# Optimization experiments

Measured on AMD Instinct MI355X. Metric: run time of the kernel, lower is better.

The kernel has to match this reference:

```python
import jax, jax.numpy as jnp
import numpy as np

LEVELS = 256          # 8-bit fake quant, quant_levels=256 in forward
SLM_CUTOFF = 0.05     # lower bound of the SLM LUT (file-loaded in original)
EPS = 1e-8


def _stats(t, pct):
    # QuantizeStats first-calibration-step semantics:
    # max = percentile(t, pct); min = t.min() if >= 0 else -max
    mx = jnp.percentile(t, pct)
    mn = jnp.min(t)
    mn = jnp.where(mn >= 0.0, mn, -mx)
    return jax.lax.stop_gradient(mn), jax.lax.stop_gradient(mx)


def _fake_quant_det(x, mn, mx, lut_min=None):
    diff = mx - mn
    q = jnp.clip(x, mn, mx)
    q = (q - mn) / (diff + EPS) * (LEVELS - 1)
    q = jnp.round(q) / (LEVELS - 1) * diff + mn
    if lut_min is not None:
        # clip positive part up to lut_min*max, negative part down to -lut_min*|min|
        pos = jax.nn.relu(q)
        neg = q - pos
        lms_p = lut_min * mx
        pos = jnp.where(pos < lms_p, lms_p, pos)
        lms_n = lut_min * jnp.abs(mn)
        neg = jnp.where(neg > -lms_n, -lms_n, neg)
        q = pos + neg
    # straight-through estimator (QuantizeValue.backward passes grad through)
    return x + jax.lax.stop_gradient(q - x)


def _fake_quant_rand(x, mn, mx, key):
    diff = mx - mn
    q = jnp.clip(x, mn, mx)
    q = (q - mn) / (diff + EPS) * (LEVELS - 1)
    noise = jax.random.uniform(key, q.shape, q.dtype) - 0.5  # stochastic rounding
    q = jnp.round(q + noise) / (LEVELS - 1) * diff + mn
    return x + jax.lax.stop_gradient(q - x)


def setup_inputs() -> dict:
    key = jax.random.key(0)
    kx, ky = jax.random.split(key)
    x = jax.random.normal(kx, (2, 4, 2048, 64), dtype=jnp.float32)
    y = jax.random.normal(ky, (2, 4, 64, 2048), dtype=jnp.float32)
    return {"x": x, "y": y}


def reference(x, y):
    # QuantizedMatmul.forward, quantize=True, training path
    x_min, x_max = _stats(x, 99.99)
    y_min, y_max = _stats(y, 98.0)
    xq = _fake_quant_det(x, x_min, x_max)
    yq = _fake_quant_det(y, y_min, y_max, SLM_CUTOFF)
    out = jnp.matmul(xq, yq)           # [B,H,M,N]
    o_min, o_max = _stats(out, 99.9999)
    return _fake_quant_rand(out, o_min, o_max, jax.random.key(1))
```

## Files before the change

### kernel.cpp

```cpp
#include <hip/hip_runtime.h>
#include <math.h>

#define CAP  (1u<<20)
#define LCAP 12288
#define LBUF 4096

typedef __attribute__((ext_vector_type(4))) float f32x4;
typedef __attribute__((ext_vector_type(8))) __bf16 bf16x8;
typedef __attribute__((ext_vector_type(8))) unsigned short u16x8;
typedef __attribute__((ext_vector_type(4))) unsigned short u16x4;

__device__ __forceinline__ unsigned f2key(float f){
  unsigned u = __float_as_uint(f);
  return (u & 0x80000000u) ? ~u : (u | 0x80000000u);
}
__device__ __forceinline__ float key2f(unsigned k){
  unsigned u = (k & 0x80000000u) ? (k & 0x7fffffffu) : ~k;
  return __uint_as_float(u);
}
__device__ __forceinline__ unsigned short f2bf(float f){
  unsigned u = __float_as_uint(f);
  u += 0x7FFFu + ((u>>16)&1u);
  return (unsigned short)(u>>16);
}

__device__ __forceinline__ void stage_bf16_tiles(
    const unsigned short* __restrict__ xq, const unsigned short* __restrict__ yqT,
    unsigned short* As, unsigned short* Bs, int brow, int bcol, int tid){
  #pragma unroll
  for (int i=0;i<4;i++){
    int u = tid + i*256;
    int row = u >> 3, ko = (u & 7) << 3;
    u16x8 v = *(const u16x8*)&xq[(size_t)(brow+row)*64 + ko];
    unsigned slot = ((unsigned)(ko>>3)) ^ ((unsigned)row & 7u);
    *(u16x8*)&As[(unsigned)row*64u + slot*8u] = v;
  }
  #pragma unroll
  for (int i=0;i<4;i++){
    int u = tid + i*256;
    int col = u >> 3, ko = (u & 7) << 3;
    u16x8 v = *(const u16x8*)&yqT[(size_t)(bcol+col)*64 + ko];
    unsigned slot = ((unsigned)(ko>>3)) ^ ((unsigned)col & 7u);
    *(u16x8*)&Bs[(unsigned)col*64u + slot*8u] = v;
  }
}

__device__ __forceinline__ void mfma_tile(
    const unsigned short* As, const unsigned short* Bs,
    f32x4 acc[2][8], int w, int lr, int lg){
  #pragma unroll
  for (int kk=0; kk<2; ++kk){
    bf16x8 a[2], bb[8];
    #pragma unroll
    for (int rt=0;rt<2;rt++){
      int row = w*32 + rt*16 + lr;
      unsigned slot = (unsigned)(kk*4 + lg) ^ ((unsigned)row & 7u);
      a[rt] = __builtin_bit_cast(bf16x8, *(const u16x8*)&As[(unsigned)row*64u + slot*8u]);
    }
    #pragma unroll
    for (int ct=0;ct<8;ct++){
      int col = ct*16 + lr;
      unsigned slot = (unsigned)(kk*4 + lg) ^ ((unsigned)col & 7u);
      bb[ct] = __builtin_bit_cast(bf16x8, *(const u16x8*)&Bs[(unsigned)col*64u + slot*8u]);
    }
    #pragma unroll
    for (int rt=0;rt<2;rt++)
      #pragma unroll
      for (int ct=0;ct<8;ct++)
        acc[rt][ct] = __builtin_amdgcn_mfma_f32_16x16x32_bf16(a[rt], bb[ct], acc[rt][ct], 0, 0, 0);
  }
}

__global__ void init_kernel(unsigned* ctrl){
  int tid = blockIdx.x*blockDim.x + threadIdx.x;
  int stride = gridDim.x*blockDim.x;
  for (int i=tid;i<8192;i+=stride) ctrl[i]=0u;
  if (tid<16) ctrl[12291+tid]=0u;
  if (tid>=16 && tid<19) ctrl[12288+(tid-16)]=0xFFFFFFFFu;
}

__global__ __launch_bounds__(256) void hist2_kernel(
    const float4* __restrict__ dA, const float4* __restrict__ dB, int n4A, int n4B,
    unsigned* __restrict__ hA, unsigned* __restrict__ hB,
    unsigned* __restrict__ mkA, unsigned* __restrict__ mkB){
  const int z = blockIdx.y;
  const float4* __restrict__ data = z ? dB : dA;
  const int n4 = z ? n4B : n4A;
  unsigned* hist = z ? hB : hA;
  unsigned* minKey = z ? mkB : mkA;
  __shared__ unsigned sh[8*4096];
  int tid = threadIdx.x;
  for (int i=tid;i<8*4096;i+=blockDim.x) sh[i]=0u;
  __syncthreads();
  const unsigned p = (unsigned)(tid & 7);
  const unsigned cp = p << 12;
  const unsigned rot = p << 2;
  unsigned lmin=0xFFFFFFFFu;
  int idx = blockIdx.x*blockDim.x + tid;
  int stride = gridDim.x*blockDim.x;
  for (int i=idx;i<n4;i+=stride){
    float4 v = data[i];
    unsigned k0=f2key(v.x), k1=f2key(v.y), k2=f2key(v.z), k3=f2key(v.w);
    atomicAdd(&sh[cp + (((k0>>20)+rot)&4095u)],1u);
    atomicAdd(&sh[cp + (((k1>>20)+rot)&4095u)],1u);
    atomicAdd(&sh[cp + (((k2>>20)+rot)&4095u)],1u);
    atomicAdd(&sh[cp + (((k3>>20)+rot)&4095u)],1u);
    lmin = min(lmin, min(min(k0,k1),min(k2,k3)));
  }
  #pragma unroll
  for (int off=32; off; off>>=1) lmin = min(lmin, __shfl_xor(lmin, off));
  if ((tid&63)==0) atomicMin(minKey, lmin);
  __syncthreads();
  for (int i=tid;i<4096;i+=blockDim.x){
    unsigned c=0;
    #pragma unroll
    for (int q=0;q<8;q++) c += sh[(q<<12) + (((unsigned)i + (q<<2))&4095u)];
    if(c) atomicAdd(&hist[i],c);
  }
}

__global__ __launch_bounds__(256) void collect2_kernel(
    const float4* __restrict__ dA, const float4* __restrict__ dB, int n4A, int n4B,
    const unsigned* __restrict__ hA, const unsigned* __restrict__ hB,
    unsigned k1A, unsigned k2A, unsigned k1B, unsigned k2B,
    float* __restrict__ candA, float* __restrict__ candB,
    unsigned* __restrict__ cntA, unsigned* __restrict__ cntB){
  const int z = blockIdx.y;
  const float4* __restrict__ data = z ? dB : dA;
  const int n4 = z ? n4B : n4A;
  const unsigned* __restrict__ hist = z ? hB : hA;
  const unsigned k1 = z ? k1B : k1A;
  const unsigned k2 = z ? k2B : k2A;
  float* cand = z ? candB : candA;
  unsigned* cnt = z ? cntB : cntA;
  __shared__ float sc[LBUF];
  __shared__ unsigned part[256];
  __shared__ unsigned sBi[2];
  __shared__ unsigned scnt, sbase;
  const int t = threadIdx.x;
  if (t==0) scnt=0u;
  unsigned h[16]; unsigned s=0;
  #pragma unroll
  for (int i=0;i<16;i++){ h[i] = hist[t*16+i]; s += h[i]; }
  part[t] = s;
  __syncthreads();
  for (int off=1; off<256; off<<=1){
    unsigned add = (t+off<256) ? part[t+off] : 0u;
    __syncthreads();
    part[t] += add;
    __syncthreads();
  }
  unsigned cum = (t<255) ? part[t+1] : 0u;
  for (int i=15;i>=0;--i){
    unsigned hh = h[i];
    unsigned b = (unsigned)(t*16+i);
    if (cum < k1 && cum + hh >= k1){ sBi[1] = b; }
    if (cum < k2 && cum + hh >= k2){ sBi[0] = b; }
    cum += hh;
  }
  __syncthreads();
  const unsigned blo = sBi[0], bhi = sBi[1];
  int idx = blockIdx.x*blockDim.x + t;
  int stride = gridDim.x*blockDim.x;
  for (int i=idx;i<n4;i+=stride){
    float4 v = data[i];
    float r[4] = {v.x,v.y,v.z,v.w};
    #pragma unroll
    for (int j=0;j<4;j++){
      unsigned b = f2key(r[j]) >> 20;
      if (b>=blo && b<=bhi){
        unsigned p = atomicAdd(&scnt,1u);
        if (p < LBUF) sc[p] = r[j];
        else { unsigned g = atomicAdd(cnt,1u); if (g<CAP) cand[g]=r[j]; }
      }
    }
  }
  __syncthreads();
  unsigned c = scnt; if (c > LBUF) c = LBUF;
  if (t==0 && c>0) sbase = atomicAdd(cnt, c);
  __syncthreads();
  for (unsigned i=t; i<c; i+=256){
    unsigned g = sbase + i;
    if (g < CAP) cand[g] = sc[i];
  }
}

__global__ __launch_bounds__(1024) void select2_kernel(
    const float* __restrict__ candA, const float* __restrict__ candB,
    const unsigned* __restrict__ cntA, const unsigned* __restrict__ cntB,
    const unsigned* __restrict__ hA, const unsigned* __restrict__ hB,
    const unsigned* __restrict__ mkA, const unsigned* __restrict__ mkB,
    unsigned k1A, unsigned k2A, unsigned k1B, unsigned k2B,
    double fracA, double fracB,
    float* __restrict__ stA, float* __restrict__ stB){
  const int z = blockIdx.x;
  const float* __restrict__ cand = z ? candB : candA;
  const unsigned* cnt = z ? cntB : cntA;
  const unsigned* __restrict__ hist_g = z ? hB : hA;
  const unsigned* mk  = z ? mkB  : mkA;
  const unsigned k1 = z ? k1B : k1A;
  const unsigned k2 = z ? k2B : k2A;
  const double frac = z ? fracB : fracA;
  float* stats = z ? stB : stA;

  __shared__ unsigned keys[LCAP];
  __shared__ unsigned histP[16*258];
  __shared__ unsigned hist[256];
  __shared__ unsigned part[256];
  __shared__ unsigned sAbove;
  __shared__ unsigned sPrefix, sK;
  __shared__ unsigned sKey[2];
  const int t = threadIdx.x;
  unsigned m = *cnt; if (m > CAP) m = CAP;
  for (unsigned i=t; i<m && i<LCAP; i+=1024) keys[i] = f2key(cand[i]);

  if (t==0) sAbove = 0u;
  if (hist_g){
    unsigned h[16]; unsigned s=0;
    if (t<256){
      #pragma unroll
      for (int i=0;i<16;i++){ h[i] = hist_g[t*16+i]; s += h[i]; }
      part[t] = s;
    }
    __syncthreads();
    for (int off=1; off<256; off<<=1){
      unsigned add = (t<256 && t+off<256) ? part[t+off] : 0u;
      __syncthreads();
      if (t<256) part[t] += add;
      __syncthreads();
    }
    if (t<256){
      unsigned cum = (t<255) ? part[t+1] : 0u;
      for (int i=15;i>=0;--i){
        unsigned hh = h[i];
        if (cum < k1 && cum + hh >= k1){ sAbove = cum; }
        cum += hh;
      }
    }
  }
  __syncthreads();
  const unsigned above = sAbove;

  for (int tg=0; tg<2; ++tg){
    unsigned k = ((tg==0) ? k1 : k2) - above;
    unsigned prefix = 0u, pmask = 0u;
    for (int s=24; s>=0; s-=8){
      for (int i=t;i<16*258;i+=1024) histP[i]=0u;
      __syncthreads();
      const unsigned base = (unsigned)(t & 15) * 258u;
      for (unsigned i=t;i<m;i+=1024){
        unsigned key = (i<LCAP) ? keys[i] : f2key(cand[i]);
        if ((key & pmask) == prefix) atomicAdd(&histP[base + ((key>>s)&255u)],1u);
      }
      __syncthreads();
      if (t<256){
        unsigned c=0;
        #pragma unroll
        for (int q=0;q<16;q++) c += histP[(unsigned)q*258u + (unsigned)t];
        hist[t] = c;
      }
      __syncthreads();
      if (t<64){
        unsigned h0=hist[t*4+0], h1=hist[t*4+1], h2=hist[t*4+2], h3=hist[t*4+3];
        unsigned g = h0+h1+h2+h3;
        unsigned acc = g;
        #pragma unroll
        for (int off=1; off<64; off<<=1){
          unsigned v = __shfl_down(acc, off);
          acc += (t+off<64) ? v : 0u;
        }
        unsigned ca3 = acc - g;
        unsigned ca2 = ca3 + h3;
        unsigned ca1 = ca2 + h2;
        unsigned ca0 = ca1 + h1;
        if (ca3<k && ca3+h3>=k){ sPrefix = prefix | ((unsigned)(4*t+3)<<s); sK = k-ca3; }
        if (ca2<k && ca2+h2>=k){ sPrefix = prefix | ((unsigned)(4*t+2)<<s); sK = k-ca2; }
        if (ca1<k && ca1+h1>=k){ sPrefix = prefix | ((unsigned)(4*t+1)<<s); sK = k-ca1; }
        if (ca0<k && ca0+h0>=k){ sPrefix = prefix | ((unsigned)(4*t+0)<<s); sK = k-ca0; }
      }
      __syncthreads();
      prefix = sPrefix;
      pmask |= (255u << s);
      k = sK;
    }
    if (t==0) sKey[tg] = prefix;
    __syncthreads();
  }
  if (t==0){
    float vhi = key2f(sKey[0]);
    float vlo = key2f(sKey[1]);
    double mx = (double)vlo + frac * ((double)vhi - (double)vlo);
    float mxf = (float)mx;
    float mnraw = key2f(*mk);
    float mnf = (mnraw >= 0.0f) ? mnraw : -mxf;
    stats[0]=mnf; stats[1]=mxf;
  }
}

__global__ __launch_bounds__(256) void prep_quant_kernel(
    const float4* __restrict__ x, const float* __restrict__ y,
    unsigned short* __restrict__ xq, unsigned short* __restrict__ yqT,
    int n4x, const float* __restrict__ stA, const float* __restrict__ stB){
  if (blockIdx.y == 0){
    const float amn=stA[0], amx=stA[1];
    const float adiff=amx-amn, adenom=adiff+1e-8f;
    int idx = blockIdx.x*256 + threadIdx.x;
    int stride = gridDim.x*256;
    for (int i=idx; i<n4x; i+=stride){
      float4 v = x[i];
      float rr[4]={v.x,v.y,v.z,v.w};
      u16x4 qv;
      #pragma unroll
      for (int j=0;j<4;j++){
        float xv = rr[j];
        float q = fminf(fmaxf(xv, amn), amx);
        q = (q - amn) / adenom * 255.0f;
        q = rintf(q);
        q = q / 255.0f * adiff + amn;
        qv[j] = f2bf(xv + (q - xv));
      }
      *(u16x4*)&xq[(size_t)i*4] = qv;
    }
  } else {
    __shared__ unsigned short Ys[64*72];
    const float bmn=stB[0], bmx=stB[1];
    const float bdiff=bmx-bmn, bdenom=bdiff+1e-8f;
    const float blp=0.05f*bmx, bln=0.05f*fabsf(bmn);
    const int blk = blockIdx.x;
    const int b = blk >> 5, ctile = blk & 31;
    const float* Y = y + (size_t)b*64*2048 + ctile*64;
    const int t = threadIdx.x;
    #pragma unroll
    for (int i=0;i<4;i++){
      int u = t + i*256;
      int k = u >> 4;
      int c4 = (u & 15) << 2;
      float4 v = *(const float4*)&Y[(size_t)k*2048 + c4];
      float rr[4]={v.x,v.y,v.z,v.w};
      #pragma unroll
      for (int j=0;j<4;j++){
        float xv = rr[j];
        float q = fminf(fmaxf(xv, bmn), bmx);
        q = (q - bmn) / bdenom * 255.0f;
        q = rintf(q);
        q = q / 255.0f * bdiff + bmn;
        float pos = fmaxf(q, 0.0f);
        float neg = q - pos;
        pos = (pos < blp) ? blp : pos;
        neg = (neg > -bln) ? -bln : neg;
        q = pos + neg;
        Ys[(c4+j)*72 + k] = f2bf(xv + (q - xv));
      }
    }
    __syncthreads();
    #pragma unroll
    for (int i=0;i<2;i++){
      int u = t + i*256;
      int col = u >> 3, ko = (u & 7) << 3;
      u16x8 v = *(const u16x8*)&Ys[col*72 + ko];
      *(u16x8*)&yqT[((size_t)b*2048 + ctile*64 + col)*64 + ko] = v;
    }
  }
}

__global__ __launch_bounds__(256) void matmul_stats_kernel(
    const unsigned short* __restrict__ xq, const unsigned short* __restrict__ yqT,
    unsigned* __restrict__ bMaxKey, unsigned* __restrict__ bMinKey){
  __shared__ unsigned short As[128*64];
  __shared__ unsigned short Bs[128*64];
  __shared__ float wred[8];
  const int b = blockIdx.z;
  xq  += (size_t)b*2048*64;
  yqT += (size_t)b*2048*64;
  const int brow = blockIdx.y*128, bcol = blockIdx.x*128;
  const int tid = threadIdx.x;
  stage_bf16_tiles(xq, yqT, As, Bs, brow, bcol, tid);
  __syncthreads();
  const int w = tid >> 6, l = tid & 63, lr = l & 15, lg = l >> 4;
  f32x4 zero = {0.f,0.f,0.f,0.f};
  f32x4 acc[2][8];
  #pragma unroll
  for (int rt=0;rt<2;rt++)
    #pragma unroll
    for (int ct=0;ct<8;ct++) acc[rt][ct]=zero;
  mfma_tile(As, Bs, acc, w, lr, lg);
  float tmx = -3.4e38f, tmn = 3.4e38f;
  #pragma unroll
  for (int rt=0;rt<2;rt++)
    #pragma unroll
    for (int ct=0;ct<8;ct++)
      #pragma unroll
      for (int g=0; g<4; g++){
        float v = acc[rt][ct][g];
        tmx = fmaxf(tmx, v);
        tmn = fminf(tmn, v);
      }
  #pragma unroll
  for (int off=32; off; off>>=1){
    tmx = fmaxf(tmx, __shfl_xor(tmx, off));
    tmn = fminf(tmn, __shfl_xor(tmn, off));
  }
  if ((tid&63)==0){ wred[tid>>6]=tmx; wred[4+(tid>>6)]=tmn; }
  __syncthreads();
  if (tid==0){
    float m4 = fmaxf(fmaxf(wred[0],wred[1]),fmaxf(wred[2],wred[3]));
    float n4 = fminf(fminf(wred[4],wred[5]),fminf(wred[6],wred[7]));
    int bid = blockIdx.x + (blockIdx.y<<4) + (blockIdx.z<<8);
    bMaxKey[bid] = f2key(m4);
    bMinKey[bid] = f2key(n4);
  }
}

__global__ __launch_bounds__(256) void thresh_kernel(
    const unsigned* __restrict__ bMaxKey, const unsigned* __restrict__ bMinKey,
    unsigned kth, unsigned* __restrict__ tkey, unsigned* __restrict__ minKeyO){
  __shared__ unsigned red[8];
  const int t = threadIdx.x;
  unsigned kz[8];
  unsigned mn = 0xFFFFFFFFu;
  #pragma unroll
  for (int i=0;i<8;i++){ kz[i] = bMaxKey[t*8+i]; mn = min(mn, bMinKey[t*8+i]); }
  #pragma unroll
  for (int off=32; off; off>>=1) mn = min(mn, __shfl_xor(mn, off));
  if ((t&63)==0) red[4+(t>>6)] = mn;
  __syncthreads();
  if (t==0) *minKeyO = min(min(red[4],red[5]),min(red[6],red[7]));
  unsigned lo=0u, hi=0xFFFFFFFFu;
  while (lo < hi){
    unsigned mid = lo + ((hi-lo)>>1) + 1u;
    unsigned c = 0;
    #pragma unroll
    for (int i=0;i<8;i++) c += (kz[i] >= mid) ? 1u : 0u;
    #pragma unroll
    for (int off=32; off; off>>=1) c += __shfl_xor(c, off);
    __syncthreads();
    if ((t&63)==0) red[t>>6] = c;
    __syncthreads();
    unsigned tot = red[0]+red[1]+red[2]+red[3];
    if (tot >= kth) lo = mid; else hi = mid - 1u;
  }
  if (t==0) *tkey = lo;
}

__global__ __launch_bounds__(256) void collect_tile_kernel(
    const unsigned short* __restrict__ xq, const unsigned short* __restrict__ yqT,
    const unsigned* __restrict__ bMaxKey, const unsigned* __restrict__ tkey,
    float* __restrict__ cand, unsigned* __restrict__ cnt){
  const unsigned T = *tkey;
  const int bid = blockIdx.x + (blockIdx.y<<4) + (blockIdx.z<<8);
  if (bMaxKey[bid] < T) return;
  __shared__ unsigned short As[128*64];
  __shared__ unsigned short Bs[128*64];
  __shared__ float sc[LBUF];
  __shared__ unsigned scnt, sbase;
  const int b = blockIdx.z;
  xq  += (size_t)b*2048*64;
  yqT += (size_t)b*2048*64;
  const int brow = blockIdx.y*128, bcol = blockIdx.x*128;
  const int tid = threadIdx.x;
  if (tid==0) scnt=0u;
  stage_bf16_tiles(xq, yqT, As, Bs, brow, bcol, tid);
  __syncthreads();
  const int w = tid >> 6, l = tid & 63, lr = l & 15, lg = l >> 4;
  f32x4 zero = {0.f,0.f,0.f,0.f};
  f32x4 acc[2][8];
  #pragma unroll
  for (int rt=0;rt<2;rt++)
    #pragma unroll
    for (int ct=0;ct<8;ct++) acc[rt][ct]=zero;
  mfma_tile(As, Bs, acc, w, lr, lg);
  #pragma unroll
  for (int rt=0;rt<2;rt++)
    #pragma unroll
    for (int ct=0;ct<8;ct++)
      #pragma unroll
      for (int g=0; g<4; g++){
        float v = acc[rt][ct][g];
        if (f2key(v) >= T){
          unsigned p = atomicAdd(&scnt,1u);
          if (p < LBUF) sc[p] = v;
          else { unsigned gg = atomicAdd(cnt,1u); if (gg<CAP) cand[gg]=v; }
        }
      }
  __syncthreads();
  unsigned c = scnt; if (c > LBUF) c = LBUF;
  if (tid==0 && c>0) sbase = atomicAdd(cnt, c);
  __syncthreads();
  for (unsigned i=tid; i<c; i+=256){
    unsigned g = sbase + i;
    if (g < CAP) cand[g] = sc[i];
  }
}

__global__ __launch_bounds__(256) void matmul_quant_kernel(
    const unsigned short* __restrict__ xq, const unsigned short* __restrict__ yqT,
    float* __restrict__ C, const float* __restrict__ stO){
  __shared__ unsigned short As[128*64];
  __shared__ unsigned short Bs[128*64];
  const float omn=stO[0], omx=stO[1];
  const float odiff=omx-omn, odenom=odiff+1e-8f;
  const int b = blockIdx.z;
  xq  += (size_t)b*2048*64;
  yqT += (size_t)b*2048*64;
  C   += (size_t)b*2048*2048;
  const int brow = blockIdx.y*128, bcol = blockIdx.x*128;
  const int tid = threadIdx.x;
  stage_bf16_tiles(xq, yqT, As, Bs, brow, bcol, tid);
  __syncthreads();
  const int w = tid >> 6, l = tid & 63, lr = l & 15, lg = l >> 4;
  f32x4 zero = {0.f,0.f,0.f,0.f};
  f32x4 acc[2][8];
  #pragma unroll
  for (int rt=0;rt<2;rt++)
    #pragma unroll
    for (int ct=0;ct<8;ct++) acc[rt][ct]=zero;
  mfma_tile(As, Bs, acc, w, lr, lg);
  #pragma unroll
  for (int rt=0;rt<2;rt++)
    #pragma unroll
    for (int ct=0;ct<8;ct++)
      #pragma unroll
      for (int g=0; g<4; g++){
        float x = acc[rt][ct][g];
        float q = fminf(fmaxf(x, omn), omx);
        q = (q - omn) / odenom * 255.0f;
        q = rintf(q);
        q = q / 255.0f * odiff + omn;
        float v = x + (q - x);
        int row = brow + w*32 + rt*16 + lg*4 + g;
        int col = bcol + ct*16 + lr;
        C[(size_t)row*2048 + col] = v;
      }
}

static void percentile_ranks(long long n, double pct, unsigned& k1, unsigned& k2, double& frac){
  double p = (double)(n - 1) * (pct / 100.0);
  double fi = floor(p);
  frac = p - fi;
  long long i0 = (long long)fi;
  k2 = (unsigned)(n - i0);
  k1 = k2 - 1u;
}

extern "C" void kernel_launch(void* const* d_in, const int* in_sizes, int n_in,
                              void* d_out, int out_size, void* d_ws, size_t ws_size,
                              hipStream_t stream) {
  const float* x = (const float*)d_in[0];
  const float* y = (const float*)d_in[1];
  float* out = (float*)d_out;
  char* ws = (char*)d_ws;

  const long long nX = (long long)in_sizes[0];
  const long long nY = (long long)in_sizes[1];
  const long long nO = (long long)out_size;
  const int nX4 = (int)(nX/4), nY4 = (int)(nY/4);

  float*    candx = (float*)(ws);
  float*    candy = (float*)(ws + (5ll<<20));
  float*    cando = (float*)(ws + (10ll<<20));
  unsigned* ctrl  = (unsigned*)(ws + (15ll<<20));
  unsigned short* xq  = (unsigned short*)(ws + (16ll<<20));
  unsigned short* yqT = (unsigned short*)(ws + (18ll<<20));
  unsigned *hx = ctrl, *hy = ctrl+4096;
  unsigned* minkey = ctrl + 12288;
  unsigned* cnt    = ctrl + 12291;
  unsigned* tkey   = ctrl + 12303;
  float* stx = (float*)(ctrl + 12304);
  float* sty = stx + 2;
  float* sto = stx + 4;
  unsigned* bMaxKey = ctrl + 12320;
  unsigned* bMinKey = ctrl + 14368;

  unsigned k1x,k2x,k1y,k2y,k1o,k2o; double fx,fy,fo;
  percentile_ranks(nX, 99.99,   k1x, k2x, fx);
  percentile_ranks(nY, 98.0,    k1y, k2y, fy);
  percentile_ranks(nO, 99.9999, k1o, k2o, fo);

  init_kernel<<<32,256,0,stream>>>(ctrl);

  hist2_kernel<<<dim3(128,2),256,0,stream>>>((const float4*)x,(const float4*)y,nX4,nY4,hx,hy,minkey+0,minkey+1);
  collect2_kernel<<<dim3(128,2),256,0,stream>>>((const float4*)x,(const float4*)y,nX4,nY4,hx,hy,
                                                k1x,k2x,k1y,k2y,candx,candy,cnt+0,cnt+1);
  select2_kernel<<<2,1024,0,stream>>>(candx,candy,cnt+0,cnt+1,hx,hy,minkey+0,minkey+1,
                                      k1x,k2x,k1y,k2y,fx,fy,stx,sty);

  prep_quant_kernel<<<dim3(256,2),256,0,stream>>>((const float4*)x, y, xq, yqT, nX4, stx, sty);

  matmul_stats_kernel<<<dim3(16,16,8),256,0,stream>>>(xq, yqT, bMaxKey, bMinKey);

  thresh_kernel<<<1,256,0,stream>>>(bMaxKey, bMinKey, k2o, tkey, minkey+2);
  collect_tile_kernel<<<dim3(16,16,8),256,0,stream>>>(xq, yqT, bMaxKey, tkey, cando, cnt+2);
  select2_kernel<<<1,1024,0,stream>>>(cando,cando,cnt+2,cnt+2,(const unsigned*)nullptr,(const unsigned*)nullptr,
                                      minkey+2,minkey+2,k1o,k2o,k1o,k2o,fo,fo,sto,sto);

  matmul_quant_kernel<<<dim3(16,16,8),256,0,stream>>>(xq, yqT, out, sto);
}
```

Before: 137.5 us.

## Fuse select and threshold kernels into producers via last-block completion counters

Drops the separate select2 and thresh kernel launches. The last finishing block of collect2, matmul_stats and collect_tile, detected with an atomic done counter and a threadfence, now runs the radix selection or threshold search itself. Candidates are stored as keys through atomics so the last block sees them coherently. It also stages the matmul_quant output through shared memory so global writes are float4 coalesced. The trade-off is that the selection now runs in a single 256-thread block instead of 1024 threads, with a smaller LDS key cache.

```diff
diff --git a/kernel.cpp b/kernel.cpp
--- a/kernel.cpp
+++ b/kernel.cpp
@@ -2,7 +2,6 @@
 #include <math.h>
 
 #define CAP  (1u<<20)
-#define LCAP 12288
 #define LBUF 4096
 
 typedef __attribute__((ext_vector_type(4))) float f32x4;
@@ -23,6 +22,7 @@
   u += 0x7FFFu + ((u>>16)&1u);
   return (unsigned short)(u>>16);
 }
+__device__ __forceinline__ unsigned aload(unsigned* p){ return atomicOr(p, 0u); }
 
 __device__ __forceinline__ void stage_bf16_tiles(
     const unsigned short* __restrict__ xq, const unsigned short* __restrict__ yqT,
@@ -71,189 +71,28 @@
   }
 }
 
-__global__ void init_kernel(unsigned* ctrl){
-  int tid = blockIdx.x*blockDim.x + threadIdx.x;
-  int stride = gridDim.x*blockDim.x;
-  for (int i=tid;i<8192;i+=stride) ctrl[i]=0u;
-  if (tid<16) ctrl[12291+tid]=0u;
-  if (tid>=16 && tid<19) ctrl[12288+(tid-16)]=0xFFFFFFFFu;
-}
-
-__global__ __launch_bounds__(256) void hist2_kernel(
-    const float4* __restrict__ dA, const float4* __restrict__ dB, int n4A, int n4B,
-    unsigned* __restrict__ hA, unsigned* __restrict__ hB,
-    unsigned* __restrict__ mkA, unsigned* __restrict__ mkB){
-  const int z = blockIdx.y;
-  const float4* __restrict__ data = z ? dB : dA;
-  const int n4 = z ? n4B : n4A;
-  unsigned* hist = z ? hB : hA;
-  unsigned* minKey = z ? mkB : mkA;
-  __shared__ unsigned sh[8*4096];
-  int tid = threadIdx.x;
-  for (int i=tid;i<8*4096;i+=blockDim.x) sh[i]=0u;
-  __syncthreads();
-  const unsigned p = (unsigned)(tid & 7);
-  const unsigned cp = p << 12;
-  const unsigned rot = p << 2;
-  unsigned lmin=0xFFFFFFFFu;
-  int idx = blockIdx.x*blockDim.x + tid;
-  int stride = gridDim.x*blockDim.x;
-  for (int i=idx;i<n4;i+=stride){
-    float4 v = data[i];
-    unsigned k0=f2key(v.x), k1=f2key(v.y), k2=f2key(v.z), k3=f2key(v.w);
-    atomicAdd(&sh[cp + (((k0>>20)+rot)&4095u)],1u);
-    atomicAdd(&sh[cp + (((k1>>20)+rot)&4095u)],1u);
-    atomicAdd(&sh[cp + (((k2>>20)+rot)&4095u)],1u);
-    atomicAdd(&sh[cp + (((k3>>20)+rot)&4095u)],1u);
-    lmin = min(lmin, min(min(k0,k1),min(k2,k3)));
-  }
-  #pragma unroll
-  for (int off=32; off; off>>=1) lmin = min(lmin, __shfl_xor(lmin, off));
-  if ((tid&63)==0) atomicMin(minKey, lmin);
-  __syncthreads();
-  for (int i=tid;i<4096;i+=blockDim.x){
-    unsigned c=0;
-    #pragma unroll
-    for (int q=0;q<8;q++) c += sh[(q<<12) + (((unsigned)i + (q<<2))&4095u)];
-    if(c) atomicAdd(&hist[i],c);
-  }
-}
-
-__global__ __launch_bounds__(256) void collect2_kernel(
-    const float4* __restrict__ dA, const float4* __restrict__ dB, int n4A, int n4B,
-    const unsigned* __restrict__ hA, const unsigned* __restrict__ hB,
-    unsigned k1A, unsigned k2A, unsigned k1B, unsigned k2B,
-    float* __restrict__ candA, float* __restrict__ candB,
-    unsigned* __restrict__ cntA, unsigned* __restrict__ cntB){
-  const int z = blockIdx.y;
-  const float4* __restrict__ data = z ? dB : dA;
-  const int n4 = z ? n4B : n4A;
-  const unsigned* __restrict__ hist = z ? hB : hA;
-  const unsigned k1 = z ? k1B : k1A;
-  const unsigned k2 = z ? k2B : k2A;
-  float* cand = z ? candB : candA;
-  unsigned* cnt = z ? cntB : cntA;
-  __shared__ float sc[LBUF];
-  __shared__ unsigned part[256];
-  __shared__ unsigned sBi[2];
-  __shared__ unsigned scnt, sbase;
+__device__ void select_radix256(
+    unsigned* candU, unsigned m, unsigned above,
+    unsigned k1, unsigned k2, double frac, float mnraw,
+    unsigned* keys, unsigned lcap,
+    unsigned* histP, unsigned* hist, float* stats){
+  __shared__ unsigned sPrefix, sK, sKey2[2];
   const int t = threadIdx.x;
-  if (t==0) scnt=0u;
-  unsigned h[16]; unsigned s=0;
-  #pragma unroll
-  for (int i=0;i<16;i++){ h[i] = hist[t*16+i]; s += h[i]; }
-  part[t] = s;
-  __syncthreads();
-  for (int off=1; off<256; off<<=1){
-    unsigned add = (t+off<256) ? part[t+off] : 0u;
-    __syncthreads();
-    part[t] += add;
-    __syncthreads();
-  }
-  unsigned cum = (t<255) ? part[t+1] : 0u;
-  for (int i=15;i>=0;--i){
-    unsigned hh = h[i];
-    unsigned b = (unsigned)(t*16+i);
-    if (cum < k1 && cum + hh >= k1){ sBi[1] = b; }
-    if (cum < k2 && cum + hh >= k2){ sBi[0] = b; }
-    cum += hh;
-  }
-  __syncthreads();
-  const unsigned blo = sBi[0], bhi = sBi[1];
-  int idx = blockIdx.x*blockDim.x + t;
-  int stride = gridDim.x*blockDim.x;
-  for (int i=idx;i<n4;i+=stride){
-    float4 v = data[i];
-    float r[4] = {v.x,v.y,v.z,v.w};
-    #pragma unroll
-    for (int j=0;j<4;j++){
-      unsigned b = f2key(r[j]) >> 20;
-      if (b>=blo && b<=bhi){
-        unsigned p = atomicAdd(&scnt,1u);
-        if (p < LBUF) sc[p] = r[j];
-        else { unsigned g = atomicAdd(cnt,1u); if (g<CAP) cand[g]=r[j]; }
-      }
-    }
-  }
-  __syncthreads();
-  unsigned c = scnt; if (c > LBUF) c = LBUF;
-  if (t==0 && c>0) sbase = atomicAdd(cnt, c);
-  __syncthreads();
-  for (unsigned i=t; i<c; i+=256){
-    unsigned g = sbase + i;
-    if (g < CAP) cand[g] = sc[i];
-  }
-}
-
-__global__ __launch_bounds__(1024) void select2_kernel(
-    const float* __restrict__ candA, const float* __restrict__ candB,
-    const unsigned* __restrict__ cntA, const unsigned* __restrict__ cntB,
-    const unsigned* __restrict__ hA, const unsigned* __restrict__ hB,
-    const unsigned* __restrict__ mkA, const unsigned* __restrict__ mkB,
-    unsigned k1A, unsigned k2A, unsigned k1B, unsigned k2B,
-    double fracA, double fracB,
-    float* __restrict__ stA, float* __restrict__ stB){
-  const int z = blockIdx.x;
-  const float* __restrict__ cand = z ? candB : candA;
-  const unsigned* cnt = z ? cntB : cntA;
-  const unsigned* __restrict__ hist_g = z ? hB : hA;
-  const unsigned* mk  = z ? mkB  : mkA;
-  const unsigned k1 = z ? k1B : k1A;
-  const unsigned k2 = z ? k2B : k2A;
-  const double frac = z ? fracB : fracA;
-  float* stats = z ? stB : stA;
-
-  __shared__ unsigned keys[LCAP];
-  __shared__ unsigned histP[16*258];
-  __shared__ unsigned hist[256];
-  __shared__ unsigned part[256];
-  __shared__ unsigned sAbove;
-  __shared__ unsigned sPrefix, sK;
-  __shared__ unsigned sKey[2];
-  const int t = threadIdx.x;
-  unsigned m = *cnt; if (m > CAP) m = CAP;
-  for (unsigned i=t; i<m && i<LCAP; i+=1024) keys[i] = f2key(cand[i]);
-
-  if (t==0) sAbove = 0u;
-  if (hist_g){
-    unsigned h[16]; unsigned s=0;
-    if (t<256){
-      #pragma unroll
-      for (int i=0;i<16;i++){ h[i] = hist_g[t*16+i]; s += h[i]; }
-      part[t] = s;
-    }
-    __syncthreads();
-    for (int off=1; off<256; off<<=1){
-      unsigned add = (t<256 && t+off<256) ? part[t+off] : 0u;
-      __syncthreads();
-      if (t<256) part[t] += add;
-      __syncthreads();
-    }
-    if (t<256){
-      unsigned cum = (t<255) ? part[t+1] : 0u;
-      for (int i=15;i>=0;--i){
-        unsigned hh = h[i];
-        if (cum < k1 && cum + hh >= k1){ sAbove = cum; }
-        cum += hh;
-      }
-    }
-  }
-  __syncthreads();
-  const unsigned above = sAbove;
-
+  for (unsigned i=t; i<m && i<lcap; i+=256) keys[i] = aload(&candU[i]);
+  __syncthreads();
   for (int tg=0; tg<2; ++tg){
     unsigned k = ((tg==0) ? k1 : k2) - above;
     unsigned prefix = 0u, pmask = 0u;
     for (int s=24; s>=0; s-=8){
-      for (int i=t;i<16*258;i+=1024) histP[i]=0u;
+      for (unsigned i=t; i<16u*258u; i+=256) histP[i]=0u;
       __syncthreads();
       const unsigned base = (unsigned)(t & 15) * 258u;
-      for (unsigned i=t;i<m;i+=1024){
-        unsigned key = (i<LCAP) ? keys[i] : f2key(cand[i]);
+      for (unsigned i=t; i<m; i+=256){
+        unsigned key = (i<lcap) ? keys[i] : aload(&candU[i]);
         if ((key & pmask) == prefix) atomicAdd(&histP[base + ((key>>s)&255u)],1u);
       }
       __syncthreads();
-      if (t<256){
+      {
         unsigned c=0;
         #pragma unroll
         for (int q=0;q<16;q++) c += histP[(unsigned)q*258u + (unsigned)t];
@@ -282,18 +121,186 @@
       prefix = sPrefix;
       pmask |= (255u << s);
       k = sK;
-    }
-    if (t==0) sKey[tg] = prefix;
+      __syncthreads();
+    }
+    if (t==0) sKey2[tg] = prefix;
     __syncthreads();
   }
   if (t==0){
-    float vhi = key2f(sKey[0]);
-    float vlo = key2f(sKey[1]);
+    float vhi = key2f(sKey2[0]);
+    float vlo = key2f(sKey2[1]);
     double mx = (double)vlo + frac * ((double)vhi - (double)vlo);
     float mxf = (float)mx;
-    float mnraw = key2f(*mk);
     float mnf = (mnraw >= 0.0f) ? mnraw : -mxf;
     stats[0]=mnf; stats[1]=mxf;
+  }
+}
+
+__device__ void thresh256(unsigned* bMaxKey, unsigned* bMinKey, unsigned kth,
+                          unsigned* tkey, unsigned* minKeyO){
+  __shared__ unsigned red[8];
+  const int t = threadIdx.x;
+  unsigned kz[8];
+  unsigned mn = 0xFFFFFFFFu;
+  #pragma unroll
+  for (int i=0;i<8;i++){ kz[i] = aload(&bMaxKey[t*8+i]); mn = min(mn, aload(&bMinKey[t*8+i])); }
+  #pragma unroll
+  for (int off=32; off; off>>=1) mn = min(mn, __shfl_xor(mn, off));
+  if ((t&63)==0) red[4+(t>>6)] = mn;
+  __syncthreads();
+  if (t==0) *minKeyO = min(min(red[4],red[5]),min(red[6],red[7]));
+  unsigned lo=0u, hi=0xFFFFFFFFu;
+  while (lo < hi){
+    unsigned mid = lo + ((hi-lo)>>1) + 1u;
+    unsigned c = 0;
+    #pragma unroll
+    for (int i=0;i<8;i++) c += (kz[i] >= mid) ? 1u : 0u;
+    #pragma unroll
+    for (int off=32; off; off>>=1) c += __shfl_xor(c, off);
+    __syncthreads();
+    if ((t&63)==0) red[t>>6] = c;
+    __syncthreads();
+    unsigned tot = red[0]+red[1]+red[2]+red[3];
+    if (tot >= kth) lo = mid; else hi = mid - 1u;
+  }
+  if (t==0) *tkey = lo;
+}
+
+__global__ void init_kernel(unsigned* ctrl){
+  int tid = blockIdx.x*blockDim.x + threadIdx.x;
+  int stride = gridDim.x*blockDim.x;
+  for (int i=tid;i<8192;i+=stride) ctrl[i]=0u;
+  if (tid<13) ctrl[12291+tid]=0u;
+  if (tid>=16 && tid<19) ctrl[12288+(tid-16)]=0xFFFFFFFFu;
+}
+
+__global__ __launch_bounds__(256) void hist2_kernel(
+    const float4* __restrict__ dA, const float4* __restrict__ dB, int n4A, int n4B,
+    unsigned* __restrict__ hA, unsigned* __restrict__ hB,
+    unsigned* __restrict__ mkA, unsigned* __restrict__ mkB){
+  const int z = blockIdx.y;
+  const float4* __restrict__ data = z ? dB : dA;
+  const int n4 = z ? n4B : n4A;
+  unsigned* hist = z ? hB : hA;
+  unsigned* minKey = z ? mkB : mkA;
+  __shared__ unsigned sh[8*4096];
+  int tid = threadIdx.x;
+  for (int i=tid;i<8*4096;i+=blockDim.x) sh[i]=0u;
+  __syncthreads();
+  const unsigned p = (unsigned)(tid & 7);
+  const unsigned cp = p << 12;
+  const unsigned rot = p << 2;
+  unsigned lmin=0xFFFFFFFFu;
+  int idx = blockIdx.x*blockDim.x + tid;
+  int stride = gridDim.x*blockDim.x;
+  for (int i=idx;i<n4;i+=stride){
+    float4 v = data[i];
+    unsigned k0=f2key(v.x), k1=f2key(v.y), k2=f2key(v.z), k3=f2key(v.w);
+    atomicAdd(&sh[cp + (((k0>>20)+rot)&4095u)],1u);
+    atomicAdd(&sh[cp + (((k1>>20)+rot)&4095u)],1u);
+    atomicAdd(&sh[cp + (((k2>>20)+rot)&4095u)],1u);
+    atomicAdd(&sh[cp + (((k3>>20)+rot)&4095u)],1u);
+    lmin = min(lmin, min(min(k0,k1),min(k2,k3)));
+  }
+  #pragma unroll
+  for (int off=32; off; off>>=1) lmin = min(lmin, __shfl_xor(lmin, off));
+  if ((tid&63)==0) atomicMin(minKey, lmin);
+  __syncthreads();
+  for (int i=tid;i<4096;i+=blockDim.x){
+    unsigned c=0;
+    #pragma unroll
+    for (int q=0;q<8;q++) c += sh[(q<<12) + (((unsigned)i + (q<<2))&4095u)];
+    if(c) atomicAdd(&hist[i],c);
+  }
+}
+
+__global__ __launch_bounds__(256) void collect2_kernel(
+    const float4* __restrict__ dA, const float4* __restrict__ dB, int n4A, int n4B,
+    const unsigned* __restrict__ hA, const unsigned* __restrict__ hB,
+    unsigned k1A, unsigned k2A, unsigned k1B, unsigned k2B,
+    double fracA, double fracB,
+    unsigned* candA, unsigned* candB,
+    unsigned* cntA, unsigned* cntB,
+    const unsigned* __restrict__ mkA, const unsigned* __restrict__ mkB,
+    unsigned* doneXY, float* stA, float* stB){
+  __shared__ unsigned S[14896];
+  unsigned* keys  = S;
+  unsigned* scU   = S;
+  unsigned* histP = S + 10240;
+  unsigned* hist  = S + 14368;
+  unsigned* part  = S + 14624;
+  __shared__ unsigned sBi1;
+  __shared__ unsigned sBi2;
+  __shared__ unsigned sAboveS;
+  __shared__ unsigned scnt, sbase;
+  __shared__ int sLast;
+  const int z = blockIdx.y;
+  const float4* __restrict__ data = z ? dB : dA;
+  const int n4 = z ? n4B : n4A;
+  const unsigned* __restrict__ hg = z ? hB : hA;
+  const unsigned k1 = z ? k1B : k1A;
+  const unsigned k2 = z ? k2B : k2A;
+  unsigned* cand = z ? candB : candA;
+  unsigned* cnt  = z ? cntB : cntA;
+  const int t = threadIdx.x;
+  if (t==0){ scnt=0u; sAboveS=0u; }
+  unsigned h[16]; unsigned s=0;
+  #pragma unroll
+  for (int i=0;i<16;i++){ h[i] = hg[t*16+i]; s += h[i]; }
+  part[t] = s;
+  __syncthreads();
+  for (int off=1; off<256; off<<=1){
+    unsigned add = (t+off<256) ? part[t+off] : 0u;
+    __syncthreads();
+    part[t] += add;
+    __syncthreads();
+  }
+  unsigned cum = (t<255) ? part[t+1] : 0u;
+  for (int i=15;i>=0;--i){
+    unsigned hh = h[i];
+    unsigned b = (unsigned)(t*16+i);
+    if (cum < k1 && cum + hh >= k1){ sBi2 = b; sAboveS = cum; }
+    if (cum < k2 && cum + hh >= k2){ sBi1 = b; }
+    cum += hh;
+  }
+  __syncthreads();
+  const unsigned blo = sBi1, bhi = sBi2;
+  int idx = blockIdx.x*blockDim.x + t;
+  int stride = gridDim.x*blockDim.x;
+  for (int i=idx;i<n4;i+=stride){
+    float4 v = data[i];
+    float r[4] = {v.x,v.y,v.z,v.w};
+    #pragma unroll
+    for (int j=0;j<4;j++){
+      unsigned key = f2key(r[j]);
+      unsigned b = key >> 20;
+      if (b>=blo && b<=bhi){
+        unsigned p = atomicAdd(&scnt,1u);
+        if (p < LBUF) scU[p] = key;
+        else { unsigned g = atomicAdd(cnt,1u); if (g<CAP) atomicExch(&cand[g], key); }
+      }
+    }
+  }
+  __syncthreads();
+  unsigned c = scnt; if (c > LBUF) c = LBUF;
+  if (t==0 && c>0) sbase = atomicAdd(cnt, c);
+  __syncthreads();
+  for (unsigned i=t; i<c; i+=256){
+    unsigned g = sbase + i;
+    if (g < CAP) atomicExch(&cand[g], scU[i]);
+  }
+  __syncthreads();
+  if (t==0){
+    __threadfence();
+    unsigned old = atomicAdd(&doneXY[z], 1u);
+    sLast = (old == gridDim.x - 1u);
+  }
+  __syncthreads();
+  if (sLast){
+    unsigned m = atomicAdd(cnt, 0u); if (m > CAP) m = CAP;
+    float mnraw = key2f(z ? *mkB : *mkA);
+    select_radix256(cand, m, sAboveS, k1, k2, z ? fracB : fracA, mnraw,
+                    keys, 10240u, histP, hist, z ? stB : stA);
   }
 }
 
@@ -365,16 +372,18 @@
 
 __global__ __launch_bounds__(256) void matmul_stats_kernel(
     const unsigned short* __restrict__ xq, const unsigned short* __restrict__ yqT,
-    unsigned* __restrict__ bMaxKey, unsigned* __restrict__ bMinKey){
+    unsigned* bMaxKey, unsigned* bMinKey,
+    unsigned* doneS, unsigned kth, unsigned* tkey, unsigned* minKeyO){
   __shared__ unsigned short As[128*64];
   __shared__ unsigned short Bs[128*64];
   __shared__ float wred[8];
+  __shared__ int sLast;
   const int b = blockIdx.z;
-  xq  += (size_t)b*2048*64;
-  yqT += (size_t)b*2048*64;
+  const unsigned short* xqb  = xq  + (size_t)b*2048*64;
+  const unsigned short* yqTb = yqT + (size_t)b*2048*64;
   const int brow = blockIdx.y*128, bcol = blockIdx.x*128;
   const int tid = threadIdx.x;
-  stage_bf16_tiles(xq, yqT, As, Bs, brow, bcol, tid);
+  stage_bf16_tiles(xqb, yqTb, As, Bs, brow, bcol, tid);
   __syncthreads();
   const int w = tid >> 6, l = tid & 63, lr = l & 15, lg = l >> 4;
   f32x4 zero = {0.f,0.f,0.f,0.f};
@@ -406,60 +415,102 @@
     float m4 = fmaxf(fmaxf(wred[0],wred[1]),fmaxf(wred[2],wred[3]));
     float n4 = fminf(fminf(wred[4],wred[5]),fminf(wred[6],wred[7]));
     int bid = blockIdx.x + (blockIdx.y<<4) + (blockIdx.z<<8);
-    bMaxKey[bid] = f2key(m4);
-    bMinKey[bid] = f2key(n4);
-  }
-}
-
-__global__ __launch_bounds__(256) void thresh_kernel(
-    const unsigned* __restrict__ bMaxKey, const unsigned* __restrict__ bMinKey,
-    unsigned kth, unsigned* __restrict__ tkey, unsigned* __restrict__ minKeyO){
-  __shared__ unsigned red[8];
-  const int t = threadIdx.x;
-  unsigned kz[8];
-  unsigned mn = 0xFFFFFFFFu;
-  #pragma unroll
-  for (int i=0;i<8;i++){ kz[i] = bMaxKey[t*8+i]; mn = min(mn, bMinKey[t*8+i]); }
-  #pragma unroll
-  for (int off=32; off; off>>=1) mn = min(mn, __shfl_xor(mn, off));
-  if ((t&63)==0) red[4+(t>>6)] = mn;
-  __syncthreads();
-  if (t==0) *minKeyO = min(min(red[4],red[5]),min(red[6],red[7]));
-  unsigned lo=0u, hi=0xFFFFFFFFu;
-  while (lo < hi){
-    unsigned mid = lo + ((hi-lo)>>1) + 1u;
-    unsigned c = 0;
-    #pragma unroll
-    for (int i=0;i<8;i++) c += (kz[i] >= mid) ? 1u : 0u;
-    #pragma unroll
-    for (int off=32; off; off>>=1) c += __shfl_xor(c, off);
-    __syncthreads();
-    if ((t&63)==0) red[t>>6] = c;
-    __syncthreads();
-    unsigned tot = red[0]+red[1]+red[2]+red[3];
-    if (tot >= kth) lo = mid; else hi = mid - 1u;
-  }
-  if (t==0) *tkey = lo;
+    atomicExch(&bMaxKey[bid], f2key(m4));
+    atomicExch(&bMinKey[bid], f2key(n4));
+    __threadfence();
+    unsigned old = atomicAdd(doneS, 1u);
+    sLast = (old == 2047u);
+  }
+  __syncthreads();
+  if (sLast) thresh256(bMaxKey, bMinKey, kth, tkey, minKeyO);
 }
 
 __global__ __launch_bounds__(256) void collect_tile_kernel(
     const unsigned short* __restrict__ xq, const unsigned short* __restrict__ yqT,
     const unsigned* __restrict__ bMaxKey, const unsigned* __restrict__ tkey,
-    float* __restrict__ cand, unsigned* __restrict__ cnt){
+    unsigned* cand, unsigned* cnt, unsigned* doneC,
+    const unsigned* __restrict__ minKeyO,
+    unsigned k1o, unsigned k2o, double fo, float* stO){
+  __shared__ unsigned S[12300];
+  unsigned short* As = (unsigned short*)S;
+  unsigned short* Bs = (unsigned short*)(S + 4096);
+  unsigned* scU   = S + 8192;
+  unsigned* keys  = S;
+  unsigned* histP = S + 4096;
+  unsigned* hist  = S + 8224;
+  __shared__ unsigned scnt, sbase;
+  __shared__ int sLast;
   const unsigned T = *tkey;
   const int bid = blockIdx.x + (blockIdx.y<<4) + (blockIdx.z<<8);
-  if (bMaxKey[bid] < T) return;
-  __shared__ unsigned short As[128*64];
-  __shared__ unsigned short Bs[128*64];
-  __shared__ float sc[LBUF];
-  __shared__ unsigned scnt, sbase;
+  const int tid = threadIdx.x;
+  if (tid==0) scnt=0u;
+  __syncthreads();
+  if (bMaxKey[bid] >= T){
+    const int b = blockIdx.z;
+    const unsigned short* xqb  = xq  + (size_t)b*2048*64;
+    const unsigned short* yqTb = yqT + (size_t)b*2048*64;
+    const int brow = blockIdx.y*128, bcol = blockIdx.x*128;
+    stage_bf16_tiles(xqb, yqTb, As, Bs, brow, bcol, tid);
+    __syncthreads();
+    const int w = tid >> 6, l = tid & 63, lr = l & 15, lg = l >> 4;
+    f32x4 zero = {0.f,0.f,0.f,0.f};
+    f32x4 acc[2][8];
+    #pragma unroll
+    for (int rt=0;rt<2;rt++)
+      #pragma unroll
+      for (int ct=0;ct<8;ct++) acc[rt][ct]=zero;
+    mfma_tile(As, Bs, acc, w, lr, lg);
+    #pragma unroll
+    for (int rt=0;rt<2;rt++)
+      #pragma unroll
+      for (int ct=0;ct<8;ct++)
+        #pragma unroll
+        for (int g=0; g<4; g++){
+          unsigned key = f2key(acc[rt][ct][g]);
+          if (key >= T){
+            unsigned p = atomicAdd(&scnt,1u);
+            if (p < LBUF) scU[p] = key;
+            else { unsigned gg = atomicAdd(cnt,1u); if (gg<CAP) atomicExch(&cand[gg], key); }
+          }
+        }
+    __syncthreads();
+    unsigned c = scnt; if (c > LBUF) c = LBUF;
+    if (tid==0 && c>0) sbase = atomicAdd(cnt, c);
+    __syncthreads();
+    for (unsigned i=tid; i<c; i+=256){
+      unsigned g = sbase + i;
+      if (g < CAP) atomicExch(&cand[g], scU[i]);
+    }
+  }
+  __syncthreads();
+  if (tid==0){
+    __threadfence();
+    unsigned old = atomicAdd(doneC, 1u);
+    sLast = (old == 2047u);
+  }
+  __syncthreads();
+  if (sLast){
+    unsigned m = atomicAdd(cnt, 0u); if (m > CAP) m = CAP;
+    float mnraw = key2f(*minKeyO);
+    select_radix256(cand, m, 0u, k1o, k2o, fo, mnraw, keys, 4096u, histP, hist, stO);
+  }
+}
+
+__global__ __launch_bounds__(256) void matmul_quant_kernel(
+    const unsigned short* __restrict__ xq, const unsigned short* __restrict__ yqT,
+    float* __restrict__ C, const float* __restrict__ stO){
+  __shared__ float smem[8704];
+  unsigned short* As = (unsigned short*)smem;
+  unsigned short* Bs = As + 8192;
+  const float omn=stO[0], omx=stO[1];
+  const float odiff=omx-omn, odenom=odiff+1e-8f;
   const int b = blockIdx.z;
-  xq  += (size_t)b*2048*64;
-  yqT += (size_t)b*2048*64;
+  const unsigned short* xqb  = xq  + (size_t)b*2048*64;
+  const unsigned short* yqTb = yqT + (size_t)b*2048*64;
+  C += (size_t)b*2048*2048;
   const int brow = blockIdx.y*128, bcol = blockIdx.x*128;
   const int tid = threadIdx.x;
-  if (tid==0) scnt=0u;
-  stage_bf16_tiles(xq, yqT, As, Bs, brow, bcol, tid);
+  stage_bf16_tiles(xqb, yqTb, As, Bs, brow, bcol, tid);
   __syncthreads();
   const int w = tid >> 6, l = tid & 63, lr = l & 15, lg = l >> 4;
   f32x4 zero = {0.f,0.f,0.f,0.f};
@@ -469,68 +520,35 @@
     #pragma unroll
     for (int ct=0;ct<8;ct++) acc[rt][ct]=zero;
   mfma_tile(As, Bs, acc, w, lr, lg);
-  #pragma unroll
-  for (int rt=0;rt<2;rt++)
-    #pragma unroll
-    for (int ct=0;ct<8;ct++)
+  __syncthreads();
+  float* Cw = smem + w*2176;
+  #pragma unroll
+  for (int h=0; h<2; ++h){
+    #pragma unroll
+    for (int rt=0;rt<2;rt++)
       #pragma unroll
-      for (int g=0; g<4; g++){
-        float v = acc[rt][ct][g];
-        if (f2key(v) >= T){
-          unsigned p = atomicAdd(&scnt,1u);
-          if (p < LBUF) sc[p] = v;
-          else { unsigned gg = atomicAdd(cnt,1u); if (gg<CAP) cand[gg]=v; }
+      for (int c2=0;c2<4;c2++){
+        int ct = h*4 + c2;
+        #pragma unroll
+        for (int g=0; g<4; g++){
+          float x = acc[rt][ct][g];
+          float q = fminf(fmaxf(x, omn), omx);
+          q = (q - omn) / odenom * 255.0f;
+          q = rintf(q);
+          q = q / 255.0f * odiff + omn;
+          Cw[(rt*16 + lg*4 + g)*68 + c2*16 + lr] = x + (q - x);
         }
       }
-  __syncthreads();
-  unsigned c = scnt; if (c > LBUF) c = LBUF;
-  if (tid==0 && c>0) sbase = atomicAdd(cnt, c);
-  __syncthreads();
-  for (unsigned i=tid; i<c; i+=256){
-    unsigned g = sbase + i;
-    if (g < CAP) cand[g] = sc[i];
-  }
-}
-
-__global__ __launch_bounds__(256) void matmul_quant_kernel(
-    const unsigned short* __restrict__ xq, const unsigned short* __restrict__ yqT,
-    float* __restrict__ C, const float* __restrict__ stO){
-  __shared__ unsigned short As[128*64];
-  __shared__ unsigned short Bs[128*64];
-  const float omn=stO[0], omx=stO[1];
-  const float odiff=omx-omn, odenom=odiff+1e-8f;
-  const int b = blockIdx.z;
-  xq  += (size_t)b*2048*64;
-  yqT += (size_t)b*2048*64;
-  C   += (size_t)b*2048*2048;
-  const int brow = blockIdx.y*128, bcol = blockIdx.x*128;
-  const int tid = threadIdx.x;
-  stage_bf16_tiles(xq, yqT, As, Bs, brow, bcol, tid);
-  __syncthreads();
-  const int w = tid >> 6, l = tid & 63, lr = l & 15, lg = l >> 4;
-  f32x4 zero = {0.f,0.f,0.f,0.f};
-  f32x4 acc[2][8];
-  #pragma unroll
-  for (int rt=0;rt<2;rt++)
-    #pragma unroll
-    for (int ct=0;ct<8;ct++) acc[rt][ct]=zero;
-  mfma_tile(As, Bs, acc, w, lr, lg);
-  #pragma unroll
-  for (int rt=0;rt<2;rt++)
-    #pragma unroll
-    for (int ct=0;ct<8;ct++)
-      #pragma unroll
-      for (int g=0; g<4; g++){
-        float x = acc[rt][ct][g];
-        float q = fminf(fmaxf(x, omn), omx);
-        q = (q - omn) / odenom * 255.0f;
-        q = rintf(q);
-        q = q / 255.0f * odiff + omn;
-        float v = x + (q - x);
-        int row = brow + w*32 + rt*16 + lg*4 + g;
-        int col = bcol + ct*16 + lr;
-        C[(size_t)row*2048 + col] = v;
-      }
+    #pragma unroll
+    for (int i=0;i<8;i++){
+      int u = l + 64*i;
+      int row = u >> 4;
+      int c4 = (u & 15) << 2;
+      float4 v4 = *(float4*)&Cw[row*68 + c4];
+      int gr = brow + w*32 + row;
+      *(float4*)&C[(size_t)gr*2048 + bcol + h*64 + c4] = v4;
+    }
+  }
 }
 
 static void percentile_ranks(long long n, double pct, unsigned& k1, unsigned& k2, double& frac){
@@ -555,15 +573,18 @@
   const long long nO = (long long)out_size;
   const int nX4 = (int)(nX/4), nY4 = (int)(nY/4);
 
-  float*    candx = (float*)(ws);
-  float*    candy = (float*)(ws + (5ll<<20));
-  float*    cando = (float*)(ws + (10ll<<20));
+  unsigned* candx = (unsigned*)(ws);
+  unsigned* candy = (unsigned*)(ws + (5ll<<20));
+  unsigned* cando = (unsigned*)(ws + (10ll<<20));
   unsigned* ctrl  = (unsigned*)(ws + (15ll<<20));
   unsigned short* xq  = (unsigned short*)(ws + (16ll<<20));
   unsigned short* yqT = (unsigned short*)(ws + (18ll<<20));
   unsigned *hx = ctrl, *hy = ctrl+4096;
   unsigned* minkey = ctrl + 12288;
   unsigned* cnt    = ctrl + 12291;
+  unsigned* doneXY = ctrl + 12294;
+  unsigned* doneS  = ctrl + 12296;
+  unsigned* doneC  = ctrl + 12297;
   unsigned* tkey   = ctrl + 12303;
   float* stx = (float*)(ctrl + 12304);
   float* sty = stx + 2;
@@ -580,18 +601,17 @@
 
   hist2_kernel<<<dim3(128,2),256,0,stream>>>((const float4*)x,(const float4*)y,nX4,nY4,hx,hy,minkey+0,minkey+1);
   collect2_kernel<<<dim3(128,2),256,0,stream>>>((const float4*)x,(const float4*)y,nX4,nY4,hx,hy,
-                                                k1x,k2x,k1y,k2y,candx,candy,cnt+0,cnt+1);
-  select2_kernel<<<2,1024,0,stream>>>(candx,candy,cnt+0,cnt+1,hx,hy,minkey+0,minkey+1,
-                                      k1x,k2x,k1y,k2y,fx,fy,stx,sty);
+                                                k1x,k2x,k1y,k2y,fx,fy,candx,candy,cnt+0,cnt+1,
+                                                minkey+0,minkey+1,doneXY,stx,sty);
 
   prep_quant_kernel<<<dim3(256,2),256,0,stream>>>((const float4*)x, y, xq, yqT, nX4, stx, sty);
 
-  matmul_stats_kernel<<<dim3(16,16,8),256,0,stream>>>(xq, yqT, bMaxKey, bMinKey);
-
-  thresh_kernel<<<1,256,0,stream>>>(bMaxKey, bMinKey, k2o, tkey, minkey+2);
-  collect_tile_kernel<<<dim3(16,16,8),256,0,stream>>>(xq, yqT, bMaxKey, tkey, cando, cnt+2);
-  select2_kernel<<<1,1024,0,stream>>>(cando,cando,cnt+2,cnt+2,(const unsigned*)nullptr,(const unsigned*)nullptr,
-                                      minkey+2,minkey+2,k1o,k2o,k1o,k2o,fo,fo,sto,sto);
+  matmul_stats_kernel<<<dim3(16,16,8),256,0,stream>>>(xq, yqT, bMaxKey, bMinKey,
+                                                      doneS, k2o, tkey, minkey+2);
+
+  collect_tile_kernel<<<dim3(16,16,8),256,0,stream>>>(xq, yqT, bMaxKey, tkey,
+                                                      cando, cnt+2, doneC, minkey+2,
+                                                      k1o, k2o, fo, sto);
 
   matmul_quant_kernel<<<dim3(16,16,8),256,0,stream>>>(xq, yqT, out, sto);
 }
```

After: 249.8 us. +81.6%, slower.
